# Kernel tuning notes

Hardware: AMD Instinct MI355X
Metric: run time of the kernel (lower is better)

## Reference

```python
import jax, jax.numpy as jnp
import numpy as np
from jax import lax

B, S, I, K = 64, 512, 50, 4
H_FC, OUT, H_R = 1024, 128, 512


def setup_inputs() -> dict:
    key = jax.random.key(0)
    ks = jax.random.split(key, 24)
    inp = {}
    inp["x"] = jax.random.normal(ks[0], (B, S, I), dtype=jnp.float32)
    # col 0 = mu, col 1 = sigma (divisor); uniform(0,1) shifted away from 0 for stability
    fp = jax.random.uniform(ks[1], (I * K, 2), dtype=jnp.float32)
    inp["fuzzy_params"] = fp.at[:, 1].add(0.5)
    # FC stack: (I*K -> H_FC), (H_FC -> H_FC) x (num_fc-2=2), (H_FC -> OUT)
    dims = [(H_FC, I * K), (H_FC, H_FC), (H_FC, H_FC), (OUT, H_FC)]
    for j, (o, i) in enumerate(dims):
        inp[f"fc{j}_w"] = jax.random.normal(ks[2 + 2 * j], (o, i), dtype=jnp.float32) * 0.02
        inp[f"fc{j}_b"] = jnp.zeros((o,), dtype=jnp.float32)
    # 2-layer Elman RNN (tanh), batch_first
    inp["w_ih0"] = jax.random.normal(ks[12], (H_R, OUT), dtype=jnp.float32) * 0.04
    inp["w_hh0"] = jax.random.normal(ks[13], (H_R, H_R), dtype=jnp.float32) * 0.04
    inp["b_ih0"] = jnp.zeros((H_R,), dtype=jnp.float32)
    inp["b_hh0"] = jnp.zeros((H_R,), dtype=jnp.float32)
    inp["w_ih1"] = jax.random.normal(ks[14], (H_R, H_R), dtype=jnp.float32) * 0.04
    inp["w_hh1"] = jax.random.normal(ks[15], (H_R, H_R), dtype=jnp.float32) * 0.04
    inp["b_ih1"] = jnp.zeros((H_R,), dtype=jnp.float32)
    inp["b_hh1"] = jnp.zeros((H_R,), dtype=jnp.float32)
    return inp


def _rnn_layer(inp, w_ih, w_hh, b_ih, b_hh):
    # inp: [B,S,D] -> [B,S,H]; precompute input projection, scan recurrence over time
    pre = jnp.einsum("bsd,hd->bsh", inp, w_ih) + b_ih + b_hh

    def step(h, x_t):
        h = jnp.tanh(x_t + h @ w_hh.T)
        return h, h

    h0 = jnp.zeros((inp.shape[0], w_hh.shape[0]), dtype=inp.dtype)
    _, ys = lax.scan(step, h0, jnp.swapaxes(pre, 0, 1))  # [S,B,H]
    return jnp.swapaxes(ys, 0, 1)


def reference(x, fuzzy_params, fc0_w, fc0_b, fc1_w, fc1_b, fc2_w, fc2_b, fc3_w, fc3_b,
              w_ih0, w_hh0, b_ih0, b_hh0, w_ih1, w_hh1, b_ih1, b_hh1):
    # Fuzzy layer: exp(-(x - mu_k)^2 / sigma_k), output ordered as [k, i] flattened
    mu = fuzzy_params[:, 0].reshape(K, I)
    sig = fuzzy_params[:, 1].reshape(K, I)
    z = jnp.exp(-((x[:, :, None, :] - mu) ** 2) / sig)  # [B,S,K,I]
    z = z.reshape(x.shape[0], x.shape[1], K * I)
    # FC stack (no nonlinearity in original)
    for w, b in ((fc0_w, fc0_b), (fc1_w, fc1_b), (fc2_w, fc2_b), (fc3_w, fc3_b)):
        z = z @ w.T + b
    # 2-layer tanh RNN
    z = _rnn_layer(z, w_ih0, w_hh0, b_ih0, b_hh0)
    z = _rnn_layer(z, w_ih1, w_hh1, b_ih1, b_hh1)
    return z
```

## Files before the change

kernel.cpp:

```cpp
#include <hip/hip_runtime.h>
#include <hip/hip_fp16.h>
#include <cstddef>


typedef _Float16 half8 __attribute__((ext_vector_type(8)));
typedef float f32x4 __attribute__((ext_vector_type(4)));
typedef float f32v4 __attribute__((ext_vector_type(4)));
typedef _Float16 v2h __attribute__((ext_vector_type(2)));

__device__ __forceinline__ void gld_lds16(const void* g, void* lds) {
  __builtin_amdgcn_global_load_lds(
      (const __attribute__((address_space(1))) unsigned int*)g,
      (__attribute__((address_space(3))) unsigned int*)lds, 16, 0, 0);
}

__global__ void fuzzy16(const float* __restrict__ x, const float* __restrict__ fp,
                        _Float16* __restrict__ z, int nrows) {
  int idx = blockIdx.x * blockDim.x + threadIdx.x;
  if (idx >= nrows * 256) return;
  int r = idx >> 8;
  int f = idx & 255;
  float v = 0.f;
  if (f < 200) {
    int i = f % 50;
    float xv = x[r * 50 + i];
    float mu = fp[2 * f];
    float sg = fp[2 * f + 1];
    float d = xv - mu;
    v = expf(-(d * d) / sg);
  }
  z[idx] = (_Float16)v;
}

__global__ void cvt_w16(const float* __restrict__ W, _Float16* __restrict__ O,
                        int rows, int kin, int kpad) {
  int idx = blockIdx.x * blockDim.x + threadIdx.x;
  if (idx >= rows * kpad) return;
  int r = idx / kpad;
  int k = idx - r * kpad;
  O[idx] = (k < kin) ? (_Float16)W[(size_t)r * kin + k] : (_Float16)0.f;
}

__global__ __launch_bounds__(256) void gemm16(
    const _Float16* __restrict__ A, const _Float16* __restrict__ W,
    const float* __restrict__ b1, const float* __restrict__ b2,
    _Float16* __restrict__ C, int M, int N, int K) {
  __shared__ _Float16 As[128 * 32];
  __shared__ _Float16 Bs[128 * 32];
  const int tid = threadIdx.x;
  const int bm = blockIdx.y * 128;
  const int bn = blockIdx.x * 128;
  const int lane = tid & 63;
  const int wv = tid >> 6;
  const int wm = (wv >> 1) * 64;
  const int wn = (wv & 1) * 64;
  const int frow = lane & 15;
  const int fk = (lane >> 4) * 8;

  const int srow = tid >> 2;
  const int scol = (tid & 3) * 16;
  const char* gA = (const char*)(A + (size_t)(bm + srow) * K) + scol;
  const char* gB = (const char*)(W + (size_t)(bn + srow) * K) + scol;
  const size_t rowstep = (size_t)64 * K * 2;
  char* lA = (char*)As + tid * 16;
  char* lB = (char*)Bs + tid * 16;

  f32x4 acc[4][4] = {};

  for (int k0 = 0; k0 < K; k0 += 32) {
    gld_lds16(gA, lA);
    gld_lds16(gA + rowstep, lA + 4096);
    gld_lds16(gB, lB);
    gld_lds16(gB + rowstep, lB + 4096);
    gA += 64;
    gB += 64;
    __syncthreads();
    half8 af[4], bf[4];
#pragma unroll
    for (int i = 0; i < 4; i++) {
      af[i] = *(const half8*)(As + (wm + i * 16 + frow) * 32 + fk);
      bf[i] = *(const half8*)(Bs + (wn + i * 16 + frow) * 32 + fk);
    }
#pragma unroll
    for (int i = 0; i < 4; i++)
#pragma unroll
      for (int j = 0; j < 4; j++)
        acc[i][j] = __builtin_amdgcn_mfma_f32_16x16x32_f16(af[i], bf[j], acc[i][j], 0, 0, 0);
    __syncthreads();
  }

  float bias[4];
#pragma unroll
  for (int j = 0; j < 4; j++) {
    int col = bn + wn + j * 16 + frow;
    bias[j] = b1[col] + (b2 ? b2[col] : 0.f);
  }
  const int r0 = (lane >> 4) * 4;
#pragma unroll
  for (int i = 0; i < 4; i++) {
#pragma unroll
    for (int r = 0; r < 4; r++) {
      int row = bm + wm + i * 16 + r0 + r;
      _Float16* Cp = C + (size_t)row * N + bn + wn + frow;
#pragma unroll
      for (int j = 0; j < 4; j++)
        Cp[j * 16] = (_Float16)(acc[i][j][r] + bias[j]);
    }
  }
}

__global__ void pack_whh_fp16(const float* __restrict__ W, float4* __restrict__ QW) {
  int idx = blockIdx.x * blockDim.x + threadIdx.x;
  if (idx >= 32768) return;
  int j4 = idx >> 9;
  int o = idx & 511;
  const float* src = W + (size_t)o * 512 + j4 * 8;
  __align__(16) __half2 p[4];
#pragma unroll
  for (int k = 0; k < 4; k++)
    p[k] = __halves2half2(__float2half(src[2 * k]), __float2half(src[2 * k + 1]));
  QW[idx] = *(const float4*)p;
}

__device__ __forceinline__ float dot2acc(float wbits, float hbits, float acc) {
#if __has_builtin(__builtin_amdgcn_fdot2)
  return __builtin_amdgcn_fdot2(__builtin_bit_cast(v2h, wbits),
                                __builtin_bit_cast(v2h, hbits), acc, false);
#else
  float2 wf = __half22float2(__builtin_bit_cast(__half2, wbits));
  float2 hf = __half22float2(__builtin_bit_cast(__half2, hbits));
  return fmaf(wf.x, hf.x, fmaf(wf.y, hf.y, acc));
#endif
}

#define FOR_WREG(X) \
  X(0) X(1) X(2) X(3) X(4) X(5) X(6) X(7) X(8) X(9) \
  X(10) X(11) X(12) X(13) X(14) X(15) X(16) X(17) X(18) X(19) \
  X(20) X(21) X(22) X(23) X(24) X(25) X(26) X(27) X(28) X(29) \
  X(30) X(31) X(32) X(33) X(34) X(35) X(36) X(37) X(38) X(39) \
  X(40) X(41) X(42) X(43) X(44) X(45) X(46) X(47) X(48)

#define NLDSG 15

__global__ __launch_bounds__(512, 2) void rnn_resident2_k(
    const _Float16* __restrict__ pre,
    const f32v4* __restrict__ QW,
    float* __restrict__ out32,
    _Float16* __restrict__ out16) {
  const int b = blockIdx.x;
  const int o = threadIdx.x;
  __shared__ f32v4 wlds[NLDSG][512];
  __shared__ __align__(16) __half hbuf[2][512];

  const f32v4* qro = QW + o;
#define DECLW(g) f32v4 w##g = qro[(g) << 9];
  FOR_WREG(DECLW)
#pragma unroll
  for (int g = 0; g < NLDSG; g++) wlds[g][o] = qro[(49 + g) << 9];

  hbuf[0][o] = __float2half(0.f);
  __syncthreads();

  const _Float16* preb = pre + (size_t)b * 262144;
  float* ob32 = out32 ? out32 + (size_t)b * 262144 : nullptr;
  _Float16* ob16 = out16 ? out16 + (size_t)b * 262144 : nullptr;

  _Float16 pcur = preb[o];
  int p = 0;
  for (int t = 0; t < 512; t++) {
    const f32v4* hs4 = (const f32v4*)hbuf[p];
    float a0 = (float)pcur;
    float a1 = 0.f, a2 = 0.f, a3 = 0.f;
    if (t < 511) pcur = preb[(t + 1) * 512 + o];

#define DOTW(g)                              \
  {                                          \
    f32v4 hq = hs4[g];                       \
    a0 = dot2acc(w##g.x, hq.x, a0);          \
    a1 = dot2acc(w##g.y, hq.y, a1);          \
    a2 = dot2acc(w##g.z, hq.z, a2);          \
    a3 = dot2acc(w##g.w, hq.w, a3);          \
  }
    FOR_WREG(DOTW)

#pragma unroll
    for (int g = 0; g < NLDSG; g++) {
      f32v4 q = wlds[g][o];
      f32v4 hq = hs4[49 + g];
      a0 = dot2acc(q.x, hq.x, a0);
      a1 = dot2acc(q.y, hq.y, a1);
      a2 = dot2acc(q.z, hq.z, a2);
      a3 = dot2acc(q.w, hq.w, a3);
    }
    float v = (a0 + a1) + (a2 + a3);
    float z = __expf(2.f * v);
    float r = __builtin_amdgcn_rcpf(z + 1.f);
    float hn = fmaf(-2.f, r, 1.f);
    hbuf[p ^ 1][o] = __float2half(hn);
    if (ob32) ob32[t * 512 + o] = hn;
    if (ob16) ob16[t * 512 + o] = (_Float16)hn;
    p ^= 1;
    __syncthreads();
  }
}

extern "C" void kernel_launch(void* const* d_in, const int* in_sizes, int n_in,
                              void* d_out, int out_size, void* d_ws, size_t ws_size,
                              hipStream_t stream) {
  const float* x     = (const float*)d_in[0];
  const float* fp    = (const float*)d_in[1];
  const float* fc0_w = (const float*)d_in[2];
  const float* fc0_b = (const float*)d_in[3];
  const float* fc1_w = (const float*)d_in[4];
  const float* fc1_b = (const float*)d_in[5];
  const float* fc2_w = (const float*)d_in[6];
  const float* fc2_b = (const float*)d_in[7];
  const float* fc3_w = (const float*)d_in[8];
  const float* fc3_b = (const float*)d_in[9];
  const float* w_ih0 = (const float*)d_in[10];
  const float* w_hh0 = (const float*)d_in[11];
  const float* b_ih0 = (const float*)d_in[12];
  const float* b_hh0 = (const float*)d_in[13];
  const float* w_ih1 = (const float*)d_in[14];
  const float* w_hh1 = (const float*)d_in[15];
  const float* b_ih1 = (const float*)d_in[16];
  const float* b_hh1 = (const float*)d_in[17];
  float* out = (float*)d_out;
  float* ws  = (float*)d_ws;

  _Float16* preH = (_Float16*)ws;
  float* U = ws + 8388608;
  _Float16* h16 = (_Float16*)U;
  _Float16* t0  = (_Float16*)U;
  float* R2 = U + 4194304;
  _Float16* t1  = (_Float16*)R2;
  _Float16* zc  = (_Float16*)R2;
  _Float16* f3  = (_Float16*)(R2 + 1048576);
  float* wbase = ws + 16777216;
  float4*   QW0   = (float4*)wbase;
  float4*   QW1   = (float4*)(wbase + 131072);
  _Float16* fc0h  = (_Float16*)(wbase + 262144);
  _Float16* fc1h  = (_Float16*)(wbase + 393216);
  _Float16* fc2h  = (_Float16*)(wbase + 917504);
  _Float16* fc3h  = (_Float16*)(wbase + 1441792);
  _Float16* wih0h = (_Float16*)(wbase + 1507328);
  _Float16* wih1h = (_Float16*)(wbase + 1540096);

  pack_whh_fp16<<<128, 256, 0, stream>>>(w_hh0, QW0);
  pack_whh_fp16<<<128, 256, 0, stream>>>(w_hh1, QW1);
  cvt_w16<<<1024, 256, 0, stream>>>(fc0_w, fc0h, 1024, 200, 256);
  cvt_w16<<<4096, 256, 0, stream>>>(fc1_w, fc1h, 1024, 1024, 1024);
  cvt_w16<<<4096, 256, 0, stream>>>(fc2_w, fc2h, 1024, 1024, 1024);
  cvt_w16<<<512, 256, 0, stream>>>(fc3_w, fc3h, 128, 1024, 1024);
  cvt_w16<<<256, 256, 0, stream>>>(w_ih0, wih0h, 512, 128, 128);
  cvt_w16<<<1024, 256, 0, stream>>>(w_ih1, wih1h, 512, 512, 512);

  const int CH = 8192;
  for (int c = 0; c < 4; c++) {
    size_t row0 = (size_t)c * CH;
    fuzzy16<<<CH, 256, 0, stream>>>(x + row0 * 50, fp, zc, CH);
    gemm16<<<dim3(8, 64), 256, 0, stream>>>(zc, fc0h, fc0_b, nullptr, t0, CH, 1024, 256);
    gemm16<<<dim3(8, 64), 256, 0, stream>>>(t0, fc1h, fc1_b, nullptr, t1, CH, 1024, 1024);
    gemm16<<<dim3(8, 64), 256, 0, stream>>>(t1, fc2h, fc2_b, nullptr, t0, CH, 1024, 1024);
    gemm16<<<dim3(1, 64), 256, 0, stream>>>(t0, fc3h, fc3_b, nullptr, f3, CH, 128, 1024);
    gemm16<<<dim3(4, 64), 256, 0, stream>>>(f3, wih0h, b_ih0, b_hh0,
                                            preH + row0 * 512, CH, 512, 128);
  }

  rnn_resident2_k<<<64, 512, 0, stream>>>(preH, (const f32v4*)QW0, nullptr, h16);
  gemm16<<<dim3(4, 256), 256, 0, stream>>>(h16, wih1h, b_ih1, b_hh1, preH, 32768, 512, 512);
  rnn_resident2_k<<<64, 512, 0, stream>>>(preH, (const f32v4*)QW1, out, nullptr);
}
```

Before: 2.100 ms.

## Split RNN recurrence matvec across waves by K-slice with LDS partial-sum reduction

The recurrent kernel is restructured so each wave owns a 64-element slice of the hidden input dimension, and each lane computes 8 output neurons over that slice. Previously each thread owned one output and read the whole h vector. Each wave now reads only its own part of h from LDS as broadcast loads, which cuts LDS traffic per step. Partial sums go through an LDS buffer and are reduced after an extra barrier, adding one more __syncthreads per timestep. The weights are split between registers (48 float4) and LDS (16 groups).

```diff
diff --git a/kernel.cpp b/kernel.cpp
--- a/kernel.cpp
+++ b/kernel.cpp
@@ -133,72 +133,100 @@
 #endif
 }
 
-#define FOR_WREG(X) \
-  X(0) X(1) X(2) X(3) X(4) X(5) X(6) X(7) X(8) X(9) \
-  X(10) X(11) X(12) X(13) X(14) X(15) X(16) X(17) X(18) X(19) \
-  X(20) X(21) X(22) X(23) X(24) X(25) X(26) X(27) X(28) X(29) \
-  X(30) X(31) X(32) X(33) X(34) X(35) X(36) X(37) X(38) X(39) \
-  X(40) X(41) X(42) X(43) X(44) X(45) X(46) X(47) X(48)
-
-#define NLDSG 15
-
-__global__ __launch_bounds__(512, 2) void rnn_resident2_k(
+#define DECLK(k)                                                           \
+  f32x4 w##k##_0 = qb[(0 << 9) + ((k) << 6)]; asm volatile("" : "+v"(w##k##_0)); \
+  f32x4 w##k##_1 = qb[(1 << 9) + ((k) << 6)]; asm volatile("" : "+v"(w##k##_1)); \
+  f32x4 w##k##_2 = qb[(2 << 9) + ((k) << 6)]; asm volatile("" : "+v"(w##k##_2)); \
+  f32x4 w##k##_3 = qb[(3 << 9) + ((k) << 6)]; asm volatile("" : "+v"(w##k##_3)); \
+  f32x4 w##k##_4 = qb[(4 << 9) + ((k) << 6)]; asm volatile("" : "+v"(w##k##_4)); \
+  f32x4 w##k##_5 = qb[(5 << 9) + ((k) << 6)]; asm volatile("" : "+v"(w##k##_5));
+
+#define DOT1(k, g)                                  \
+  acc##k = dot2acc(w##k##_##g.x, hq.x, acc##k);     \
+  acc##k = dot2acc(w##k##_##g.y, hq.y, acc##k);     \
+  acc##k = dot2acc(w##k##_##g.z, hq.z, acc##k);     \
+  acc##k = dot2acc(w##k##_##g.w, hq.w, acc##k);
+
+#define DOTG(g)                         \
+  {                                     \
+    f32v4 hq = hs4[w8 + (g)];           \
+    DOT1(0, g) DOT1(1, g) DOT1(2, g)    \
+    DOT1(3, g) DOT1(4, g) DOT1(5, g)    \
+    DOT1(6, g) DOT1(7, g)               \
+  }
+
+#define DOTLK(gp, k)                                \
+  {                                                 \
+    f32v4 q = wl[((gp) << 9) + ((k) << 6)];         \
+    acc##k = dot2acc(q.x, hq.x, acc##k);            \
+    acc##k = dot2acc(q.y, hq.y, acc##k);            \
+    acc##k = dot2acc(q.z, hq.z, acc##k);            \
+    acc##k = dot2acc(q.w, hq.w, acc##k);            \
+  }
+
+#define DOTL(gp)                                    \
+  {                                                 \
+    f32v4 hq = hs4[w8 + 6 + (gp)];                  \
+    DOTLK(gp, 0) DOTLK(gp, 1) DOTLK(gp, 2)          \
+    DOTLK(gp, 3) DOTLK(gp, 4) DOTLK(gp, 5)          \
+    DOTLK(gp, 6) DOTLK(gp, 7)                       \
+  }
+
+__global__ __launch_bounds__(512) __attribute__((amdgpu_waves_per_eu(2, 2)))
+void rnn_wavej_k(
     const _Float16* __restrict__ pre,
     const f32v4* __restrict__ QW,
     float* __restrict__ out32,
     _Float16* __restrict__ out16) {
   const int b = blockIdx.x;
-  const int o = threadIdx.x;
-  __shared__ f32v4 wlds[NLDSG][512];
+  const int tid = threadIdx.x;
+  const int w = tid >> 6;
+  const int l = tid & 63;
+  const int w8 = w << 3;
+
+  __shared__ f32v4 wlds[16][512];
+  __shared__ float psum[8][512];
   __shared__ __align__(16) __half hbuf[2][512];
 
-  const f32v4* qro = QW + o;
-#define DECLW(g) f32v4 w##g = qro[(g) << 9];
-  FOR_WREG(DECLW)
-#pragma unroll
-  for (int g = 0; g < NLDSG; g++) wlds[g][o] = qro[(49 + g) << 9];
-
-  hbuf[0][o] = __float2half(0.f);
+  const f32v4* qb = QW + ((size_t)(w8) << 9) + l;
+  DECLK(0) DECLK(1) DECLK(2) DECLK(3) DECLK(4) DECLK(5) DECLK(6) DECLK(7)
+
+  f32v4* wl = &wlds[w << 1][l];
+#pragma unroll
+  for (int gp = 0; gp < 2; gp++)
+#pragma unroll
+    for (int k = 0; k < 8; k++)
+      wl[(gp << 9) + (k << 6)] = qb[((6 + gp) << 9) + (k << 6)];
+
+  hbuf[0][tid] = __float2half(0.f);
   __syncthreads();
 
   const _Float16* preb = pre + (size_t)b * 262144;
   float* ob32 = out32 ? out32 + (size_t)b * 262144 : nullptr;
   _Float16* ob16 = out16 ? out16 + (size_t)b * 262144 : nullptr;
 
-  _Float16 pcur = preb[o];
+  _Float16 pcur = preb[tid];
   int p = 0;
   for (int t = 0; t < 512; t++) {
     const f32v4* hs4 = (const f32v4*)hbuf[p];
-    float a0 = (float)pcur;
-    float a1 = 0.f, a2 = 0.f, a3 = 0.f;
-    if (t < 511) pcur = preb[(t + 1) * 512 + o];
-
-#define DOTW(g)                              \
-  {                                          \
-    f32v4 hq = hs4[g];                       \
-    a0 = dot2acc(w##g.x, hq.x, a0);          \
-    a1 = dot2acc(w##g.y, hq.y, a1);          \
-    a2 = dot2acc(w##g.z, hq.z, a2);          \
-    a3 = dot2acc(w##g.w, hq.w, a3);          \
-  }
-    FOR_WREG(DOTW)
-
-#pragma unroll
-    for (int g = 0; g < NLDSG; g++) {
-      f32v4 q = wlds[g][o];
-      f32v4 hq = hs4[49 + g];
-      a0 = dot2acc(q.x, hq.x, a0);
-      a1 = dot2acc(q.y, hq.y, a1);
-      a2 = dot2acc(q.z, hq.z, a2);
-      a3 = dot2acc(q.w, hq.w, a3);
-    }
-    float v = (a0 + a1) + (a2 + a3);
-    float z = __expf(2.f * v);
+    float acc0 = 0.f, acc1 = 0.f, acc2 = 0.f, acc3 = 0.f;
+    float acc4 = 0.f, acc5 = 0.f, acc6 = 0.f, acc7 = 0.f;
+    DOTG(0) DOTG(1) DOTG(2) DOTG(3) DOTG(4) DOTG(5)
+    DOTL(0) DOTL(1)
+    float* ps = &psum[w][l];
+    ps[0] = acc0;   ps[64] = acc1;  ps[128] = acc2; ps[192] = acc3;
+    ps[256] = acc4; ps[320] = acc5; ps[384] = acc6; ps[448] = acc7;
+    __syncthreads();
+    float s = (float)pcur;
+    if (t < 511) pcur = preb[(t + 1) * 512 + tid];
+    s += psum[0][tid] + psum[1][tid] + psum[2][tid] + psum[3][tid] +
+         psum[4][tid] + psum[5][tid] + psum[6][tid] + psum[7][tid];
+    float z = __expf(2.f * s);
     float r = __builtin_amdgcn_rcpf(z + 1.f);
     float hn = fmaf(-2.f, r, 1.f);
-    hbuf[p ^ 1][o] = __float2half(hn);
-    if (ob32) ob32[t * 512 + o] = hn;
-    if (ob16) ob16[t * 512 + o] = (_Float16)hn;
+    hbuf[p ^ 1][tid] = __float2half(hn);
+    if (ob32) ob32[t * 512 + tid] = hn;
+    if (ob16) ob16[t * 512 + tid] = (_Float16)hn;
     p ^= 1;
     __syncthreads();
   }
@@ -267,7 +295,7 @@
                                             preH + row0 * 512, CH, 512, 128);
   }
 
-  rnn_resident2_k<<<64, 512, 0, stream>>>(preH, (const f32v4*)QW0, nullptr, h16);
+  rnn_wavej_k<<<64, 512, 0, stream>>>(preH, (const f32v4*)QW0, nullptr, h16);
   gemm16<<<dim3(4, 256), 256, 0, stream>>>(h16, wih1h, b_ih1, b_hh1, preH, 32768, 512, 512);
-  rnn_resident2_k<<<64, 512, 0, stream>>>(preH, (const f32v4*)QW1, out, nullptr);
-}
+  rnn_wavej_k<<<64, 512, 0, stream>>>(preH, (const f32v4*)QW1, out, nullptr);
+}
```

Result: no change. 2.115 ms (+0.7%).

## Compute two hidden outputs per thread in RNN kernel with 256-thread blocks

Applied to the files above, without the earlier changes.

The recurrent kernel now launches 256 threads per batch block, each computing two output neurons. Each thread keeps 96 weight vectors in registers (48 per output) and the remaining 16 per output in a swizzled LDS layout. Every h vector loaded from LDS now feeds two outputs, halving LDS reads of h per FMA and the number of waves taking part in the per-step barrier. The cost is very high register pressure, which could cause spills, and fewer waves per CU to hide latency.

```diff
diff --git a/kernel.cpp b/kernel.cpp
--- a/kernel.cpp
+++ b/kernel.cpp
@@ -133,72 +133,102 @@
 #endif
 }
 
-#define FOR_WREG(X) \
-  X(0) X(1) X(2) X(3) X(4) X(5) X(6) X(7) X(8) X(9) \
-  X(10) X(11) X(12) X(13) X(14) X(15) X(16) X(17) X(18) X(19) \
-  X(20) X(21) X(22) X(23) X(24) X(25) X(26) X(27) X(28) X(29) \
-  X(30) X(31) X(32) X(33) X(34) X(35) X(36) X(37) X(38) X(39) \
-  X(40) X(41) X(42) X(43) X(44) X(45) X(46) X(47) X(48)
-
-#define NLDSG 15
-
-__global__ __launch_bounds__(512, 2) void rnn_resident2_k(
+#define FORG48(X) \
+  X(0) X(1) X(2) X(3) X(4) X(5) X(6) X(7) \
+  X(8) X(9) X(10) X(11) X(12) X(13) X(14) X(15) \
+  X(16) X(17) X(18) X(19) X(20) X(21) X(22) X(23) \
+  X(24) X(25) X(26) X(27) X(28) X(29) X(30) X(31) \
+  X(32) X(33) X(34) X(35) X(36) X(37) X(38) X(39) \
+  X(40) X(41) X(42) X(43) X(44) X(45) X(46) X(47)
+
+#define DECLW(g)                                                        \
+  f32x4 wa##g = qA[(g) << 9]; asm volatile("" : "+v"(wa##g));           \
+  f32x4 wb##g = qB[(g) << 9]; asm volatile("" : "+v"(wb##g));
+
+#define DOTRG(g)                                       \
+  {                                                    \
+    f32v4 hq = hs4[g];                                 \
+    aA0 = dot2acc(wa##g.x, hq.x, aA0);                 \
+    aA1 = dot2acc(wa##g.y, hq.y, aA1);                 \
+    aA2 = dot2acc(wa##g.z, hq.z, aA2);                 \
+    aA3 = dot2acc(wa##g.w, hq.w, aA3);                 \
+    aB0 = dot2acc(wb##g.x, hq.x, aB0);                 \
+    aB1 = dot2acc(wb##g.y, hq.y, aB1);                 \
+    aB2 = dot2acc(wb##g.z, hq.z, aB2);                 \
+    aB3 = dot2acc(wb##g.w, hq.w, aB3);                 \
+  }
+
+__global__ __launch_bounds__(256, 1) void rnn_full_k(
     const _Float16* __restrict__ pre,
     const f32v4* __restrict__ QW,
     float* __restrict__ out32,
     _Float16* __restrict__ out16) {
   const int b = blockIdx.x;
-  const int o = threadIdx.x;
-  __shared__ f32v4 wlds[NLDSG][512];
+  const int o0 = threadIdx.x;
+  const int o1 = o0 + 256;
+
+  __shared__ f32v4 wlds[512][16];
   __shared__ __align__(16) __half hbuf[2][512];
 
-  const f32v4* qro = QW + o;
-#define DECLW(g) f32v4 w##g = qro[(g) << 9];
-  FOR_WREG(DECLW)
-#pragma unroll
-  for (int g = 0; g < NLDSG; g++) wlds[g][o] = qro[(49 + g) << 9];
-
-  hbuf[0][o] = __float2half(0.f);
+  const f32v4* qA = QW + o0;
+  const f32v4* qB = QW + o1;
+  FORG48(DECLW)
+
+  const int sw = o0 & 15;
+#pragma unroll
+  for (int gi = 0; gi < 16; gi++) {
+    wlds[o0][gi ^ sw] = qA[(48 + gi) << 9];
+    wlds[o1][gi ^ sw] = qB[(48 + gi) << 9];
+  }
+  hbuf[0][o0] = __float2half(0.f);
+  hbuf[0][o1] = __float2half(0.f);
   __syncthreads();
 
   const _Float16* preb = pre + (size_t)b * 262144;
   float* ob32 = out32 ? out32 + (size_t)b * 262144 : nullptr;
   _Float16* ob16 = out16 ? out16 + (size_t)b * 262144 : nullptr;
 
-  _Float16 pcur = preb[o];
+  _Float16 pA = preb[o0], pB = preb[o1];
   int p = 0;
   for (int t = 0; t < 512; t++) {
     const f32v4* hs4 = (const f32v4*)hbuf[p];
-    float a0 = (float)pcur;
-    float a1 = 0.f, a2 = 0.f, a3 = 0.f;
-    if (t < 511) pcur = preb[(t + 1) * 512 + o];
-
-#define DOTW(g)                              \
-  {                                          \
-    f32v4 hq = hs4[g];                       \
-    a0 = dot2acc(w##g.x, hq.x, a0);          \
-    a1 = dot2acc(w##g.y, hq.y, a1);          \
-    a2 = dot2acc(w##g.z, hq.z, a2);          \
-    a3 = dot2acc(w##g.w, hq.w, a3);          \
-  }
-    FOR_WREG(DOTW)
-
-#pragma unroll
-    for (int g = 0; g < NLDSG; g++) {
-      f32v4 q = wlds[g][o];
-      f32v4 hq = hs4[49 + g];
-      a0 = dot2acc(q.x, hq.x, a0);
-      a1 = dot2acc(q.y, hq.y, a1);
-      a2 = dot2acc(q.z, hq.z, a2);
-      a3 = dot2acc(q.w, hq.w, a3);
-    }
-    float v = (a0 + a1) + (a2 + a3);
-    float z = __expf(2.f * v);
-    float r = __builtin_amdgcn_rcpf(z + 1.f);
-    float hn = fmaf(-2.f, r, 1.f);
-    hbuf[p ^ 1][o] = __float2half(hn);
-    if (ob32) ob32[t * 512 + o] = hn;
-    if (ob16) ob16[t * 512 + o] = (_Float16)hn;
+    float aA0 = (float)pA, aA1 = 0.f, aA2 = 0.f, aA3 = 0.f;
+    float aB0 = (float)pB, aB1 = 0.f, aB2 = 0.f, aB3 = 0.f;
+    FORG48(DOTRG)
+#pragma unroll
+    for (int gi = 0; gi < 16; gi++) {
+      f32v4 hq = hs4[48 + gi];
+      f32v4 qa = wlds[o0][gi ^ sw];
+      f32v4 qb = wlds[o1][gi ^ sw];
+      aA0 = dot2acc(qa.x, hq.x, aA0);
+      aA1 = dot2acc(qa.y, hq.y, aA1);
+      aA2 = dot2acc(qa.z, hq.z, aA2);
+      aA3 = dot2acc(qa.w, hq.w, aA3);
+      aB0 = dot2acc(qb.x, hq.x, aB0);
+      aB1 = dot2acc(qb.y, hq.y, aB1);
+      aB2 = dot2acc(qb.z, hq.z, aB2);
+      aB3 = dot2acc(qb.w, hq.w, aB3);
+    }
+    if (t < 511) {
+      pA = preb[(t + 1) * 512 + o0];
+      pB = preb[(t + 1) * 512 + o1];
+    }
+    float vA = (aA0 + aA1) + (aA2 + aA3);
+    float vB = (aB0 + aB1) + (aB2 + aB3);
+    float zA = __expf(2.f * vA);
+    float hA = fmaf(-2.f, __builtin_amdgcn_rcpf(zA + 1.f), 1.f);
+    float zB = __expf(2.f * vB);
+    float hB = fmaf(-2.f, __builtin_amdgcn_rcpf(zB + 1.f), 1.f);
+    hbuf[p ^ 1][o0] = __float2half(hA);
+    hbuf[p ^ 1][o1] = __float2half(hB);
+    if (ob32) {
+      ob32[t * 512 + o0] = hA;
+      ob32[t * 512 + o1] = hB;
+    }
+    if (ob16) {
+      ob16[t * 512 + o0] = (_Float16)hA;
+      ob16[t * 512 + o1] = (_Float16)hB;
+    }
     p ^= 1;
     __syncthreads();
   }
@@ -267,7 +297,7 @@
                                             preH + row0 * 512, CH, 512, 128);
   }
 
-  rnn_resident2_k<<<64, 512, 0, stream>>>(preH, (const f32v4*)QW0, nullptr, h16);
+  rnn_full_k<<<64, 256, 0, stream>>>(preH, (const f32v4*)QW0, nullptr, h16);
   gemm16<<<dim3(4, 256), 256, 0, stream>>>(h16, wih1h, b_ih1, b_hh1, preH, 32768, 512, 512);
-  rnn_resident2_k<<<64, 512, 0, stream>>>(preH, (const f32v4*)QW1, out, nullptr);
-}
+  rnn_full_k<<<64, 256, 0, stream>>>(preH, (const f32v4*)QW1, out, nullptr);
+}
```

After: 4.329 ms. 2.06x slower.
